# Performance work log

Measured on AMD Instinct MI355X. Metric: run time of the kernel, lower is better.

## Reference

```python
import jax, jax.numpy as jnp
import numpy as np

GROUP_SIZE = 128
OUT_F, IN_F = 4096, 4096
B, S = 4, 2048


@jax.custom_vjp
def ste_sign(x):
    return jnp.sign(x)

def _ste_fwd(x):
    return jnp.sign(x), None

def _ste_bwd(_, g):
    return (g,)  # straight-through: identity gradient

ste_sign.defvjp(_ste_fwd, _ste_bwd)


def setup_inputs() -> dict:
    key = jax.random.key(0)
    k1, k2, k3 = jax.random.split(key, 3)
    x = jax.random.normal(k1, (B, S, IN_F), dtype=jnp.float32)
    # sign weights are +/-1.0 (zeros mapped to +1, as in the torch init)
    sw = jnp.sign(jax.random.normal(k2, (OUT_F, IN_F), dtype=jnp.float32))
    sign_weights = jnp.where(sw == 0, 1.0, sw)
    # frozen per-group scales (mean |w| per group of 128); positive values
    scales = jax.random.uniform(k3, (OUT_F * IN_F // GROUP_SIZE,), dtype=jnp.float32,
                                minval=0.005, maxval=0.05)
    return {"x": x, "sign_weights": sign_weights, "scales": scales}


def reference(x, sign_weights, scales):
    # binary = sign(sign_weights) with STE (identity grad)
    binary = ste_sign(sign_weights)
    # expand per-group scales: repeat each scale GROUP_SIZE times, view as (out, in)
    scale_mat = jnp.repeat(scales, GROUP_SIZE).reshape(OUT_F, IN_F)
    weight = binary * scale_mat  # [out_f, in_f]
    # F.linear(x, weight) = x @ weight.T
    return jnp.einsum('bsi,oi->bso', x, weight.astype(x.dtype))
```

## Files before the change

kernel.cpp:

```cpp
#include <hip/hip_runtime.h>

#define K_DIM 4096
#define N_DIM 4096
#define M_DIM 8192

typedef __bf16 bf16;
typedef __attribute__((ext_vector_type(8))) __bf16 bf16x8;
typedef __attribute__((ext_vector_type(4))) float f32x4;
typedef __attribute__((ext_vector_type(8))) unsigned short u16x8;

__device__ inline unsigned short f2bf(float f) {
    unsigned u = __builtin_bit_cast(unsigned, f);
    u += 0x7fffu + ((u >> 16) & 1u);
    return (unsigned short)(u >> 16);
}

__global__ __launch_bounds__(256) void cvt_x_kernel(const float* __restrict__ x,
                                                    unsigned short* __restrict__ o) {
    const size_t i = (size_t)blockIdx.x * 256 + threadIdx.x;
    const float4* p = (const float4*)x + i * 2;
    float4 a = p[0], b = p[1];
    u16x8 v;
    v[0] = f2bf(a.x); v[1] = f2bf(a.y); v[2] = f2bf(a.z); v[3] = f2bf(a.w);
    v[4] = f2bf(b.x); v[5] = f2bf(b.y); v[6] = f2bf(b.z); v[7] = f2bf(b.w);
    *((u16x8*)o + i) = v;
}

__global__ __launch_bounds__(256) void wprep_kernel(const float* __restrict__ sw,
                                                    const float* __restrict__ scales,
                                                    unsigned short* __restrict__ o) {
    const size_t i = (size_t)blockIdx.x * 256 + threadIdx.x;
    const float s = scales[i >> 4];
    const float4* p = (const float4*)sw + i * 2;
    float4 a = p[0], b = p[1];
    u16x8 v;
    v[0] = f2bf(a.x * s); v[1] = f2bf(a.y * s); v[2] = f2bf(a.z * s); v[3] = f2bf(a.w * s);
    v[4] = f2bf(b.x * s); v[5] = f2bf(b.y * s); v[6] = f2bf(b.z * s); v[7] = f2bf(b.w * s);
    *((u16x8*)o + i) = v;
}

__device__ inline void gll16(const bf16* g, bf16* l) {
    __builtin_amdgcn_global_load_lds(
        (const __attribute__((address_space(1))) void*)g,
        (__attribute__((address_space(3))) void*)l, 16, 0, 0);
}

__global__ __launch_bounds__(256) void gemm_bt_kernel(const bf16* __restrict__ A,
                                                      const bf16* __restrict__ W,
                                                      float* __restrict__ C) {
    __shared__ bf16 As[128 * 64];
    __shared__ bf16 Bs[128 * 64];

    const int t = threadIdx.x;
    const int m0 = blockIdx.y * 128;
    const int n0 = blockIdx.x * 128;
    const int lane = t & 63;
    const int w = t >> 6;
    const int wm = (w >> 1) * 64;
    const int wn = (w & 1) * 64;
    const int lr = lane & 15;
    const int lq = lane >> 4;

    f32x4 acc[4][4] = {};

    const int srow = t >> 3;
    const int scol = (t & 7) ^ (srow & 7);
    const bf16* ga = A + (size_t)(m0 + srow) * K_DIM + scol * 8;
    const bf16* gb = W + (size_t)(n0 + srow) * K_DIM + scol * 8;
    bf16* la = As + t * 8;
    bf16* lb = Bs + t * 8;

    const int c0 = lq ^ (lr & 7);
    const bf16* pa0 = As + (wm + lr) * 64 + c0 * 8;
    const bf16* pb0 = Bs + (wn + lr) * 64 + c0 * 8;
    const bf16* pa1 = As + (wm + lr) * 64 + (c0 ^ 4) * 8;
    const bf16* pb1 = Bs + (wn + lr) * 64 + (c0 ^ 4) * 8;

    for (int kb = 0; kb < K_DIM; kb += 64) {
#pragma unroll
        for (int j = 0; j < 4; ++j)
            gll16(ga + kb + (size_t)(32 * j) * K_DIM, la + j * 2048);
#pragma unroll
        for (int j = 0; j < 4; ++j)
            gll16(gb + kb + (size_t)(32 * j) * K_DIM, lb + j * 2048);
        __syncthreads();

        bf16x8 af[4], bfr[4];
#pragma unroll
        for (int i = 0; i < 4; ++i) af[i] = *(const bf16x8*)(pa0 + i * 16 * 64);
#pragma unroll
        for (int i = 0; i < 4; ++i) bfr[i] = *(const bf16x8*)(pb0 + i * 16 * 64);
#pragma unroll
        for (int mi = 0; mi < 4; ++mi)
#pragma unroll
            for (int ni = 0; ni < 4; ++ni)
                acc[mi][ni] = __builtin_amdgcn_mfma_f32_16x16x32_bf16(
                    af[mi], bfr[ni], acc[mi][ni], 0, 0, 0);
#pragma unroll
        for (int i = 0; i < 4; ++i) af[i] = *(const bf16x8*)(pa1 + i * 16 * 64);
#pragma unroll
        for (int i = 0; i < 4; ++i) bfr[i] = *(const bf16x8*)(pb1 + i * 16 * 64);
#pragma unroll
        for (int mi = 0; mi < 4; ++mi)
#pragma unroll
            for (int ni = 0; ni < 4; ++ni)
                acc[mi][ni] = __builtin_amdgcn_mfma_f32_16x16x32_bf16(
                    af[mi], bfr[ni], acc[mi][ni], 0, 0, 0);
        __syncthreads();
    }

    float* Cb = C + (size_t)(m0 + wm) * N_DIM + n0 + wn;
#pragma unroll
    for (int mi = 0; mi < 4; ++mi)
#pragma unroll
        for (int ni = 0; ni < 4; ++ni)
#pragma unroll
            for (int r = 0; r < 4; ++r)
                Cb[(size_t)(mi * 16 + lq * 4 + r) * N_DIM + ni * 16 + lr] = acc[mi][ni][r];
}

extern "C" void kernel_launch(void* const* d_in, const int* in_sizes, int n_in,
                              void* d_out, int out_size, void* d_ws, size_t ws_size,
                              hipStream_t stream) {
    const float* x      = (const float*)d_in[0];
    const float* sw     = (const float*)d_in[1];
    const float* scales = (const float*)d_in[2];
    float* out = (float*)d_out;

    bf16* Abf = (bf16*)d_ws;
    bf16* Wbf = (bf16*)((char*)d_ws + (size_t)M_DIM * K_DIM * 2);

    cvt_x_kernel<<<(M_DIM * (size_t)K_DIM) / 8 / 256, 256, 0, stream>>>(x, (unsigned short*)Abf);
    wprep_kernel<<<(N_DIM * (size_t)K_DIM) / 8 / 256, 256, 0, stream>>>(sw, scales, (unsigned short*)Wbf);

    dim3 grid(N_DIM / 128, M_DIM / 128);
    gemm_bt_kernel<<<grid, 256, 0, stream>>>(Abf, Wbf, out);
}
```

Baseline: 539.7 us.

## Enlarge GEMM tile to 256x128 with 32x32 MFMA and merge prep kernels

Each GEMM block now computes a 256x128 output tile, and each wave covers 128x64 using 32x32x16 bf16 MFMA instead of 16x16x32. This raises arithmetic intensity per LDS and global load and halves the grid. The two conversion kernels are merged into one launch to save a launch and a tail. The cost is more LDS (48KB), many more accumulator registers per thread with launch_bounds set to 2 blocks/CU, and fewer blocks to fill the CUs.

```diff
diff --git a/kernel.cpp b/kernel.cpp
--- a/kernel.cpp
+++ b/kernel.cpp
@@ -6,7 +6,7 @@
 
 typedef __bf16 bf16;
 typedef __attribute__((ext_vector_type(8))) __bf16 bf16x8;
-typedef __attribute__((ext_vector_type(4))) float f32x4;
+typedef __attribute__((ext_vector_type(16))) float f32x16;
 typedef __attribute__((ext_vector_type(8))) unsigned short u16x8;
 
 __device__ inline unsigned short f2bf(float f) {
@@ -15,28 +15,30 @@
     return (unsigned short)(u >> 16);
 }
 
-__global__ __launch_bounds__(256) void cvt_x_kernel(const float* __restrict__ x,
-                                                    unsigned short* __restrict__ o) {
-    const size_t i = (size_t)blockIdx.x * 256 + threadIdx.x;
-    const float4* p = (const float4*)x + i * 2;
-    float4 a = p[0], b = p[1];
-    u16x8 v;
-    v[0] = f2bf(a.x); v[1] = f2bf(a.y); v[2] = f2bf(a.z); v[3] = f2bf(a.w);
-    v[4] = f2bf(b.x); v[5] = f2bf(b.y); v[6] = f2bf(b.z); v[7] = f2bf(b.w);
-    *((u16x8*)o + i) = v;
-}
-
-__global__ __launch_bounds__(256) void wprep_kernel(const float* __restrict__ sw,
-                                                    const float* __restrict__ scales,
-                                                    unsigned short* __restrict__ o) {
-    const size_t i = (size_t)blockIdx.x * 256 + threadIdx.x;
-    const float s = scales[i >> 4];
-    const float4* p = (const float4*)sw + i * 2;
-    float4 a = p[0], b = p[1];
-    u16x8 v;
-    v[0] = f2bf(a.x * s); v[1] = f2bf(a.y * s); v[2] = f2bf(a.z * s); v[3] = f2bf(a.w * s);
-    v[4] = f2bf(b.x * s); v[5] = f2bf(b.y * s); v[6] = f2bf(b.z * s); v[7] = f2bf(b.w * s);
-    *((u16x8*)o + i) = v;
+__global__ __launch_bounds__(256) void prep_kernel(const float* __restrict__ x,
+                                                   const float* __restrict__ sw,
+                                                   const float* __restrict__ scales,
+                                                   unsigned short* __restrict__ oA,
+                                                   unsigned short* __restrict__ oW) {
+    const int b = blockIdx.x;
+    if (b < 16384) {
+        const size_t i = (size_t)b * 256 + threadIdx.x;
+        const float4* p = (const float4*)x + i * 2;
+        float4 a = p[0], c = p[1];
+        u16x8 v;
+        v[0] = f2bf(a.x); v[1] = f2bf(a.y); v[2] = f2bf(a.z); v[3] = f2bf(a.w);
+        v[4] = f2bf(c.x); v[5] = f2bf(c.y); v[6] = f2bf(c.z); v[7] = f2bf(c.w);
+        *((u16x8*)oA + i) = v;
+    } else {
+        const size_t i = (size_t)(b - 16384) * 256 + threadIdx.x;
+        const float s = scales[i >> 4];
+        const float4* p = (const float4*)sw + i * 2;
+        float4 a = p[0], c = p[1];
+        u16x8 v;
+        v[0] = f2bf(a.x * s); v[1] = f2bf(a.y * s); v[2] = f2bf(a.z * s); v[3] = f2bf(a.w * s);
+        v[4] = f2bf(c.x * s); v[5] = f2bf(c.y * s); v[6] = f2bf(c.z * s); v[7] = f2bf(c.w * s);
+        *((u16x8*)oW + i) = v;
+    }
 }
 
 __device__ inline void gll16(const bf16* g, bf16* l) {
@@ -45,23 +47,23 @@
         (__attribute__((address_space(3))) void*)l, 16, 0, 0);
 }
 
-__global__ __launch_bounds__(256) void gemm_bt_kernel(const bf16* __restrict__ A,
-                                                      const bf16* __restrict__ W,
-                                                      float* __restrict__ C) {
-    __shared__ bf16 As[128 * 64];
+__global__ __launch_bounds__(256, 2) void gemm_bt_kernel(const bf16* __restrict__ A,
+                                                         const bf16* __restrict__ W,
+                                                         float* __restrict__ C) {
+    __shared__ bf16 As[256 * 64];
     __shared__ bf16 Bs[128 * 64];
 
     const int t = threadIdx.x;
-    const int m0 = blockIdx.y * 128;
+    const int m0 = blockIdx.y * 256;
     const int n0 = blockIdx.x * 128;
     const int lane = t & 63;
     const int w = t >> 6;
-    const int wm = (w >> 1) * 64;
+    const int wm = (w >> 1) * 128;
     const int wn = (w & 1) * 64;
-    const int lr = lane & 15;
-    const int lq = lane >> 4;
+    const int ln = lane & 31;
+    const int hl = lane >> 5;
 
-    f32x4 acc[4][4] = {};
+    f32x16 acc[4][2] = {};
 
     const int srow = t >> 3;
     const int scol = (t & 7) ^ (srow & 7);
@@ -70,42 +72,37 @@
     bf16* la = As + t * 8;
     bf16* lb = Bs + t * 8;
 
-    const int c0 = lq ^ (lr & 7);
-    const bf16* pa0 = As + (wm + lr) * 64 + c0 * 8;
-    const bf16* pb0 = Bs + (wn + lr) * 64 + c0 * 8;
-    const bf16* pa1 = As + (wm + lr) * 64 + (c0 ^ 4) * 8;
-    const bf16* pb1 = Bs + (wn + lr) * 64 + (c0 ^ 4) * 8;
+    int co[4];
+#pragma unroll
+    for (int ks = 0; ks < 4; ++ks) co[ks] = ((ks * 2 + hl) ^ (ln & 7)) * 8;
+    const bf16* paRow = As + (wm + ln) * 64;
+    const bf16* pbRow = Bs + (wn + ln) * 64;
 
     for (int kb = 0; kb < K_DIM; kb += 64) {
 #pragma unroll
-        for (int j = 0; j < 4; ++j)
+        for (int j = 0; j < 8; ++j)
             gll16(ga + kb + (size_t)(32 * j) * K_DIM, la + j * 2048);
 #pragma unroll
         for (int j = 0; j < 4; ++j)
             gll16(gb + kb + (size_t)(32 * j) * K_DIM, lb + j * 2048);
         __syncthreads();
 
-        bf16x8 af[4], bfr[4];
 #pragma unroll
-        for (int i = 0; i < 4; ++i) af[i] = *(const bf16x8*)(pa0 + i * 16 * 64);
+        for (int ks = 0; ks < 4; ++ks) {
+            bf16x8 af[4], bfr[2];
 #pragma unroll
-        for (int i = 0; i < 4; ++i) bfr[i] = *(const bf16x8*)(pb0 + i * 16 * 64);
+            for (int mi = 0; mi < 4; ++mi)
+                af[mi] = *(const bf16x8*)(paRow + mi * 2048 + co[ks]);
 #pragma unroll
-        for (int mi = 0; mi < 4; ++mi)
+            for (int ni = 0; ni < 2; ++ni)
+                bfr[ni] = *(const bf16x8*)(pbRow + ni * 2048 + co[ks]);
 #pragma unroll
-            for (int ni = 0; ni < 4; ++ni)
-                acc[mi][ni] = __builtin_amdgcn_mfma_f32_16x16x32_bf16(
-                    af[mi], bfr[ni], acc[mi][ni], 0, 0, 0);
+            for (int mi = 0; mi < 4; ++mi)
 #pragma unroll
-        for (int i = 0; i < 4; ++i) af[i] = *(const bf16x8*)(pa1 + i * 16 * 64);
-#pragma unroll
-        for (int i = 0; i < 4; ++i) bfr[i] = *(const bf16x8*)(pb1 + i * 16 * 64);
-#pragma unroll
-        for (int mi = 0; mi < 4; ++mi)
-#pragma unroll
-            for (int ni = 0; ni < 4; ++ni)
-                acc[mi][ni] = __builtin_amdgcn_mfma_f32_16x16x32_bf16(
-                    af[mi], bfr[ni], acc[mi][ni], 0, 0, 0);
+                for (int ni = 0; ni < 2; ++ni)
+                    acc[mi][ni] = __builtin_amdgcn_mfma_f32_32x32x16_bf16(
+                        af[mi], bfr[ni], acc[mi][ni], 0, 0, 0);
+        }
         __syncthreads();
     }
 
@@ -113,10 +110,12 @@
 #pragma unroll
     for (int mi = 0; mi < 4; ++mi)
 #pragma unroll
-        for (int ni = 0; ni < 4; ++ni)
+        for (int ni = 0; ni < 2; ++ni)
 #pragma unroll
-            for (int r = 0; r < 4; ++r)
-                Cb[(size_t)(mi * 16 + lq * 4 + r) * N_DIM + ni * 16 + lr] = acc[mi][ni][r];
+            for (int r = 0; r < 16; ++r) {
+                const int row = mi * 32 + (r & 3) + 8 * (r >> 2) + 4 * hl;
+                Cb[(size_t)row * N_DIM + ni * 32 + ln] = acc[mi][ni][r];
+            }
 }
 
 extern "C" void kernel_launch(void* const* d_in, const int* in_sizes, int n_in,
@@ -130,9 +129,9 @@
     bf16* Abf = (bf16*)d_ws;
     bf16* Wbf = (bf16*)((char*)d_ws + (size_t)M_DIM * K_DIM * 2);
 
-    cvt_x_kernel<<<(M_DIM * (size_t)K_DIM) / 8 / 256, 256, 0, stream>>>(x, (unsigned short*)Abf);
-    wprep_kernel<<<(N_DIM * (size_t)K_DIM) / 8 / 256, 256, 0, stream>>>(sw, scales, (unsigned short*)Wbf);
+    prep_kernel<<<24576, 256, 0, stream>>>(x, sw, scales,
+                                           (unsigned short*)Abf, (unsigned short*)Wbf);
 
-    dim3 grid(N_DIM / 128, M_DIM / 128);
+    dim3 grid(N_DIM / 128, M_DIM / 256);
     gemm_bt_kernel<<<grid, 256, 0, stream>>>(Abf, Wbf, out);
 }
```

Measured after the change: 517.8 us. -4.1%, faster.
